# Kernel optimization log

Hardware: AMD Instinct MI355X
Metric: run time of the kernel (lower is better)

## Reference

```python
import jax, jax.numpy as jnp
import numpy as np
from jax import lax

B, T, VC, VB, DC, DB, H, C = 32, 512, 12000, 400000, 128, 128, 256, 32


def setup_inputs() -> dict:
    key = jax.random.key(0)
    ks = jax.random.split(key, 16)
    seq_len = jax.random.randint(ks[0], (B,), T // 2, T + 1)
    pos = jnp.arange(T)[None, :]
    mask = pos < seq_len[:, None]
    chars = jnp.where(mask, jax.random.randint(ks[1], (B, T), 1, VC), 0)
    bigrams = jnp.where(mask, jax.random.randint(ks[2], (B, T), 1, VB), 0)
    target = jnp.where(mask, jax.random.randint(ks[3], (B, T), 0, C), 0)
    s = lambda k, shape, scale: jax.random.normal(k, shape, jnp.float32) * scale
    D = DC + DB
    return dict(
        chars=chars, bigrams=bigrams, seq_len=seq_len, target=target,
        char_table=s(ks[4], (VC, DC), 0.1),
        bigram_table=s(ks[5], (VB, DB), 0.1),
        Wi_f=s(ks[6], (D, 4 * H), 0.05), Wh_f=s(ks[7], (H, 4 * H), 0.05),
        b_f=jnp.zeros((4 * H,), jnp.float32),
        Wi_b=s(ks[8], (D, 4 * H), 0.05), Wh_b=s(ks[9], (H, 4 * H), 0.05),
        b_b=jnp.zeros((4 * H,), jnp.float32),
        out_W=s(ks[10], (2 * H, C), 0.05), out_b=jnp.zeros((C,), jnp.float32),
        trans=s(ks[11], (C, C), 0.1),
        start_trans=s(ks[12], (C,), 0.1), end_trans=s(ks[13], (C,), 0.1),
    )


def _lstm_dir(x_t, m_t, Wi, Wh, b, reverse):
    # x_t: [T,B,D], m_t: [T,B,1]; masked carry emulates pack_padded_sequence
    Hh = Wh.shape[0]
    Bb = x_t.shape[1]

    def step(carry, inp):
        h, c = carry
        x, m = inp
        g = x @ Wi + h @ Wh + b  # [B,4H], torch gate order i,f,g,o
        i, f, gg, o = jnp.split(g, 4, axis=-1)
        c_new = jax.nn.sigmoid(f) * c + jax.nn.sigmoid(i) * jnp.tanh(gg)
        h_new = jax.nn.sigmoid(o) * jnp.tanh(c_new)
        h = jnp.where(m, h_new, h)
        c = jnp.where(m, c_new, c)
        return (h, c), h

    init = (jnp.zeros((Bb, Hh), x_t.dtype), jnp.zeros((Bb, Hh), x_t.dtype))
    _, hs = lax.scan(step, init, (x_t, m_t), reverse=reverse)
    return hs  # [T,B,H]


def reference(chars, bigrams, seq_len, target, char_table, bigram_table,
              Wi_f, Wh_f, b_f, Wi_b, Wh_b, b_b, out_W, out_b,
              trans, start_trans, end_trans):
    mask = chars != 0  # [B,T]
    emb = jnp.concatenate([char_table[chars], bigram_table[bigrams]], axis=-1)  # [B,T,D]
    x_t = jnp.transpose(emb, (1, 0, 2))          # [T,B,D]
    m_t = mask.T[..., None]                       # [T,B,1]
    hf = _lstm_dir(x_t, m_t, Wi_f, Wh_f, b_f, False)
    hb = _lstm_dir(x_t, m_t, Wi_b, Wh_b, b_b, True)
    feats = jnp.concatenate([hf, hb], axis=-1)    # [T,B,2H]
    logits = jax.nn.log_softmax(feats @ out_W + out_b, axis=-1)  # [T,B,C]
    mt = mask.T  # [T,B]

    # CRF normalizer (forward algorithm, include_start_end_trans=True)
    alpha0 = logits[0] + start_trans[None, :]

    def step(alpha, inp):
        emit, m = inp
        new = jax.nn.logsumexp(alpha[:, :, None] + trans[None] + emit[:, None, :], axis=1)
        return jnp.where(m[:, None], new, alpha), None

    alpha, _ = lax.scan(step, alpha0, (logits[1:], mt[1:]))
    normalizer = jax.nn.logsumexp(alpha + end_trans[None, :], axis=1)  # [B]

    # gold path score
    lg = jnp.transpose(logits, (1, 0, 2))  # [B,T,C]
    emit = jnp.where(mask, jnp.take_along_axis(lg, target[..., None], axis=-1)[..., 0], 0.0)
    tr = jnp.where(mask[:, 1:], trans[target[:, :-1], target[:, 1:]], 0.0)
    last_idx = jnp.sum(mask, axis=-1).astype(jnp.int32) - 1
    last_tag = jnp.take_along_axis(target, last_idx[:, None], axis=1)[:, 0]
    gold = emit.sum(-1) + tr.sum(-1) + start_trans[target[:, 0]] + end_trans[last_tag]

    return normalizer - gold  # per-sample CRF negative log-likelihood, [B]
```

## Files before the change

kernel.cpp:

```cpp
#include <hip/hip_runtime.h>
#include <cstdint>
#include <cstddef>

typedef unsigned short u16;
typedef unsigned int u32;
typedef unsigned long long u64;

typedef short short8 __attribute__((ext_vector_type(8)));
typedef float floatx4 __attribute__((ext_vector_type(4)));

#define O_EMB    0ull
#define O_XG     8388608ull
#define O_HS     75497472ull
#define O_HST    92274688ull
#define O_LOGITS 92340224ull
#define O_WIT    94437504ull
#define O_OUTW   95486080ull
#define O_FLAGS  95518848ull
#define WS_NEED  95520896ull

__device__ __forceinline__ u16 f2bf(float x) {
    u32 u = __float_as_uint(x);
    u += 0x7fffu + ((u >> 16) & 1u);
    return (u16)(u >> 16);
}
__device__ __forceinline__ float bf2f(u16 v) { return __uint_as_float(((u32)v) << 16); }
__device__ __forceinline__ float sigm(float x) { return 1.0f / (1.0f + __expf(-x)); }
__device__ __forceinline__ float tanh_f(float x) {
    x = fminf(30.0f, fmaxf(-30.0f, x));
    float e = __expf(-2.0f * x);
    return (1.0f - e) / (1.0f + e);
}

__global__ __launch_bounds__(256) void k_init(u32* hstate_u32, int* flags) {
    int i = blockIdx.x * 256 + threadIdx.x;
    if (i < 16384) hstate_u32[i] = 0u;
    if (i < 512) flags[i] = 0;
}

__global__ __launch_bounds__(256) void k0_prep(const float* __restrict__ Wi_f, const float* __restrict__ Wi_b,
                                               const float* __restrict__ out_W,
                                               u16* __restrict__ WiT, u16* __restrict__ outWb) {
    int id = blockIdx.x * 256 + threadIdx.x;
    if (id < 524288) {
        int d = id >> 18;
        int rem = id & 262143;
        int k = rem >> 10;
        int n = rem & 1023;
        const float* Wi = d ? Wi_b : Wi_f;
        WiT[(size_t)d * 262144 + (size_t)n * 256 + k] = f2bf(Wi[(size_t)k * 1024 + n]);
    } else {
        int id2 = id - 524288;
        outWb[id2] = f2bf(out_W[id2]);
    }
}

__global__ __launch_bounds__(256) void k1_embed(const int* __restrict__ chars, const int* __restrict__ bigrams,
                                                const float* __restrict__ ct, const float* __restrict__ bt,
                                                u16* __restrict__ emb) {
    int idx = blockIdx.x * 256 + threadIdx.x;
    int r = idx >> 7;
    int p2 = (idx & 127) << 1;
    int t = r >> 5, b = r & 31;
    const float* src;
    if (p2 < 128) src = ct + (size_t)chars[b * 512 + t] * 128 + p2;
    else          src = bt + (size_t)bigrams[b * 512 + t] * 128 + (p2 - 128);
    float2 v = *(const float2*)(const void*)src;
    u32 pk = (u32)f2bf(v.x) | ((u32)f2bf(v.y) << 16);
    *(u32*)(void*)(emb + (size_t)r * 256 + p2) = pk;
}

__global__ __launch_bounds__(256) void k2_gemm(const u16* __restrict__ emb, const u16* __restrict__ WiT,
                                               const float* __restrict__ b_f, const float* __restrict__ b_b,
                                               u16* __restrict__ xg) {
    int mbase = blockIdx.x * 64;
    int nbase = blockIdx.y * 64;
    int d = blockIdx.z;
    const u16* Bt = WiT + (size_t)d * 262144;
    const float* bias = d ? b_b : b_f;
    u16* xgd = xg + (size_t)d * 16777216ull;
    int tid = threadIdx.x;
    int wv = tid >> 6, l = tid & 63, lm = l & 15, lq = l >> 4;
    floatx4 acc[4] = {{0,0,0,0},{0,0,0,0},{0,0,0,0},{0,0,0,0}};
    int arow = mbase + wv * 16 + lm;
#pragma unroll
    for (int kc = 0; kc < 8; ++kc) {
        int k0 = kc * 32 + lq * 8;
        short8 a = *(const short8*)(const void*)(emb + (size_t)arow * 256 + k0);
#pragma unroll
        for (int nt = 0; nt < 4; ++nt) {
            short8 bb = *(const short8*)(const void*)(Bt + (size_t)(nbase + nt * 16 + lm) * 256 + k0);
            acc[nt] = __builtin_amdgcn_mfma_f32_16x16x32_bf16(a, bb, acc[nt], 0, 0, 0);
        }
    }
#pragma unroll
    for (int nt = 0; nt < 4; ++nt) {
        int n = nbase + nt * 16 + lm;
        float bv = bias[n];
#pragma unroll
        for (int r = 0; r < 4; ++r) {
            int rr = mbase + wv * 16 + lq * 4 + r;
            xgd[(size_t)rr * 1024 + n] = f2bf(acc[nt][r] + bv);
        }
    }
}

__global__ __launch_bounds__(256) void k3_lstm(const u16* __restrict__ xg, const float* __restrict__ Wh_f,
                                               const float* __restrict__ Wh_b, const int* __restrict__ seq_len,
                                               u16* __restrict__ hstate, u16* __restrict__ hs,
                                               int* __restrict__ flags) {
    int bid = blockIdx.x;
    int dir = bid >> 4;
    int w = bid & 15;
    const float* Wh = dir ? Wh_b : Wh_f;
    const u16* xgd = xg + (size_t)dir * 16777216ull;
    u16* hsd = hs + (size_t)dir * 4194304ull;
    __shared__ u16 lds_w[64 * 264];
    __shared__ float gate_lds[32 * 68];
    int tid = threadIdx.x;

    for (int it = 0; it < 64; ++it) {
        int e = it * 256 + tid;
        int p = e & 63;
        int k = e >> 6;
        int gcol = (p >> 4) * 256 + w * 16 + (p & 15);
        lds_w[p * 264 + k] = f2bf(Wh[(size_t)k * 1024 + gcol]);
    }
    int bcell = tid >> 3, uu = tid & 7, c0 = uu * 2;
    int L = seq_len[bcell];
    float cst0 = 0.0f, cst1 = 0.0f;
    int wv = tid >> 6, l = tid & 63, lm = l & 15, lq = l >> 4, mt = wv & 1, nh = wv >> 1;
    int* myflags = flags + dir * 256;
    __syncthreads();

    for (int s = 0; s < 512; ++s) {
        int t = dir ? (511 - s) : s;
        u32 xgv[4];
        const u16* xrow = xgd + ((size_t)(t * 32 + bcell)) * 1024 + w * 16 + c0;
#pragma unroll
        for (int g = 0; g < 4; ++g) xgv[g] = *(const u32*)(const void*)(xrow + g * 256);

        if (s > 0) {
            if (tid < 64) {
                for (;;) {
                    int v = (tid < 16)
                        ? __hip_atomic_load(&myflags[tid * 16], __ATOMIC_RELAXED, __HIP_MEMORY_SCOPE_AGENT)
                        : 0x7fffffff;
                    if (__ballot(v >= s) == ~0ull) break;
                    __builtin_amdgcn_s_sleep(1);
                }
            }
            __syncthreads();
            __builtin_amdgcn_sched_barrier(0);
        }
        const u64* hbq = (const u64*)(const void*)(hstate + ((size_t)(dir * 2 + (s & 1))) * 8192);
        int arowh = mt * 16 + lm;
        u64 aq[16];
#pragma unroll
        for (int kc = 0; kc < 8; ++kc) {
            size_t qi = (size_t)arowh * 64 + (size_t)kc * 8 + lq * 2;
            aq[2 * kc]     = __hip_atomic_load(hbq + qi,     __ATOMIC_RELAXED, __HIP_MEMORY_SCOPE_AGENT);
            aq[2 * kc + 1] = __hip_atomic_load(hbq + qi + 1, __ATOMIC_RELAXED, __HIP_MEMORY_SCOPE_AGENT);
        }
        floatx4 acc0 = {0,0,0,0}, acc1 = {0,0,0,0};
#pragma unroll
        for (int kc = 0; kc < 8; ++kc) {
            union { u64 q[2]; short8 s8; } ua;
            ua.q[0] = aq[2 * kc];
            ua.q[1] = aq[2 * kc + 1];
            int k0 = kc * 32 + lq * 8;
            short8 b0 = *(const short8*)(const void*)&lds_w[(nh * 32 + lm) * 264 + k0];
            acc0 = __builtin_amdgcn_mfma_f32_16x16x32_bf16(ua.s8, b0, acc0, 0, 0, 0);
            short8 b1 = *(const short8*)(const void*)&lds_w[(nh * 32 + 16 + lm) * 264 + k0];
            acc1 = __builtin_amdgcn_mfma_f32_16x16x32_bf16(ua.s8, b1, acc1, 0, 0, 0);
        }
#pragma unroll
        for (int r = 0; r < 4; ++r) {
            int b2 = mt * 16 + lq * 4 + r;
            gate_lds[b2 * 68 + nh * 32 + lm] = acc0[r];
            gate_lds[b2 * 68 + nh * 32 + 16 + lm] = acc1[r];
        }
        __syncthreads();
        float hv0, hv1;
#pragma unroll
        for (int r = 0; r < 2; ++r) {
            int cc = c0 + r;
            float gi = gate_lds[bcell * 68 + cc]      + bf2f((u16)(xgv[0] >> (16 * r)));
            float gf = gate_lds[bcell * 68 + 16 + cc] + bf2f((u16)(xgv[1] >> (16 * r)));
            float gg = gate_lds[bcell * 68 + 32 + cc] + bf2f((u16)(xgv[2] >> (16 * r)));
            float go = gate_lds[bcell * 68 + 48 + cc] + bf2f((u16)(xgv[3] >> (16 * r)));
            float ig = sigm(gi), fg = sigm(gf), gt = tanh_f(gg), og = sigm(go);
            float cs = r ? cst1 : cst0;
            float cn = fg * cs + ig * gt;
            float hn = og * tanh_f(cn);
            if (dir && t >= L) { cn = cs; hn = 0.0f; }
            if (r) { cst1 = cn; hv1 = hn; } else { cst0 = cn; hv0 = hn; }
        }
        u32 hpack = (u32)f2bf(hv0) | ((u32)f2bf(hv1) << 16);
        u32* hbn = (u32*)(void*)(hstate + ((size_t)(dir * 2 + ((s + 1) & 1))) * 8192 + bcell * 256 + w * 16 + c0);
        __hip_atomic_store(hbn, hpack, __ATOMIC_RELAXED, __HIP_MEMORY_SCOPE_AGENT);
        __syncthreads();
        if (tid == 0) __hip_atomic_store(&myflags[w * 16], s + 1, __ATOMIC_RELAXED, __HIP_MEMORY_SCOPE_AGENT);
        *(u32*)(void*)(hsd + ((size_t)(t * 32 + bcell)) * 256 + w * 16 + c0) = hpack;
    }
}

__global__ __launch_bounds__(256) void k4_proj(const u16* __restrict__ hs, const u16* __restrict__ outWb,
                                               const float* __restrict__ out_b, float* __restrict__ logits) {
    int r = blockIdx.x * 8 + (threadIdx.x >> 5);
    int n = threadIdx.x & 31;
    const u16* hf = hs + (size_t)r * 256;
    const u16* hbk = hs + 4194304ull + (size_t)r * 256;
    float acc = out_b[n];
#pragma unroll 4
    for (int k = 0; k < 256; k += 2) {
        u32 hv = *(const u32*)(const void*)(hf + k);
        acc += bf2f((u16)hv) * bf2f(outWb[k * 32 + n]);
        acc += bf2f((u16)(hv >> 16)) * bf2f(outWb[(k + 1) * 32 + n]);
    }
#pragma unroll 4
    for (int k = 0; k < 256; k += 2) {
        u32 hv = *(const u32*)(const void*)(hbk + k);
        acc += bf2f((u16)hv) * bf2f(outWb[(256 + k) * 32 + n]);
        acc += bf2f((u16)(hv >> 16)) * bf2f(outWb[(257 + k) * 32 + n]);
    }
    float m = acc;
#pragma unroll
    for (int d2 = 16; d2 >= 1; d2 >>= 1) m = fmaxf(m, __shfl_xor(m, d2, 32));
    float s = __expf(acc - m);
#pragma unroll
    for (int d2 = 16; d2 >= 1; d2 >>= 1) s += __shfl_xor(s, d2, 32);
    logits[(size_t)r * 32 + n] = acc - m - __logf(s);
}

__global__ __launch_bounds__(256) void k5_crf(const float* __restrict__ logits, const int* __restrict__ target,
                                              const int* __restrict__ seq_len, const float* __restrict__ trans,
                                              const float* __restrict__ start_trans, const float* __restrict__ end_trans,
                                              float* __restrict__ out) {
    int b = blockIdx.x;
    int tid = threadIdx.x;
    int L = seq_len[b];
    __shared__ float alpha[32];
    __shared__ float red[4];
    __shared__ float goldsh;

    float part = 0.0f;
    for (int t = tid; t < 512; t += 256) {
        if (t < L) {
            int tg = target[b * 512 + t];
            part += logits[((size_t)(t * 32 + b)) * 32 + tg];
            if (t >= 1) part += trans[target[b * 512 + t - 1] * 32 + tg];
        }
    }
#pragma unroll
    for (int d2 = 32; d2 >= 1; d2 >>= 1) part += __shfl_xor(part, d2, 64);
    if ((tid & 63) == 0) red[tid >> 6] = part;
    __syncthreads();
    if (tid == 0) {
        float g = red[0] + red[1] + red[2] + red[3];
        g += start_trans[target[b * 512]];
        g += end_trans[target[b * 512 + L - 1]];
        goldsh = g;
    }
    if (tid < 32) alpha[tid] = logits[(size_t)b * 32 + tid] + start_trans[tid];
    __syncthreads();

    int j = tid >> 3, uu = tid & 7;
    float tr4[4];
#pragma unroll
    for (int r = 0; r < 4; ++r) tr4[r] = trans[(uu * 4 + r) * 32 + j];
    float e_next = logits[((size_t)(32 + b)) * 32 + j];
    for (int t = 1; t < 512; ++t) {
        float e = e_next;
        if (t < 511) e_next = logits[((size_t)((t + 1) * 32 + b)) * 32 + j];
        float a0 = alpha[uu * 4 + 0] + tr4[0];
        float a1 = alpha[uu * 4 + 1] + tr4[1];
        float a2 = alpha[uu * 4 + 2] + tr4[2];
        float a3 = alpha[uu * 4 + 3] + tr4[3];
        float m = fmaxf(fmaxf(a0, a1), fmaxf(a2, a3));
#pragma unroll
        for (int d2 = 4; d2 >= 1; d2 >>= 1) m = fmaxf(m, __shfl_xor(m, d2, 8));
        float ss = __expf(a0 - m) + __expf(a1 - m) + __expf(a2 - m) + __expf(a3 - m);
#pragma unroll
        for (int d2 = 4; d2 >= 1; d2 >>= 1) ss += __shfl_xor(ss, d2, 8);
        float nv = e + m + __logf(ss);
        __syncthreads();
        if (uu == 0 && t < L) alpha[j] = nv;
        __syncthreads();
    }
    if (tid < 32) {
        float v = alpha[tid] + end_trans[tid];
        float m = v;
#pragma unroll
        for (int d2 = 16; d2 >= 1; d2 >>= 1) m = fmaxf(m, __shfl_xor(m, d2, 32));
        float s2 = __expf(v - m);
#pragma unroll
        for (int d2 = 16; d2 >= 1; d2 >>= 1) s2 += __shfl_xor(s2, d2, 32);
        if (tid == 0) out[b] = m + __logf(s2) - goldsh;
    }
}

extern "C" void kernel_launch(void* const* d_in, const int* in_sizes, int n_in,
                              void* d_out, int out_size, void* d_ws, size_t ws_size,
                              hipStream_t stream) {
    if (ws_size < WS_NEED) return;
    const int* chars = (const int*)d_in[0];
    const int* bigrams = (const int*)d_in[1];
    const int* seq_len = (const int*)d_in[2];
    const int* target = (const int*)d_in[3];
    const float* char_table = (const float*)d_in[4];
    const float* bigram_table = (const float*)d_in[5];
    const float* Wi_f = (const float*)d_in[6];
    const float* Wh_f = (const float*)d_in[7];
    const float* b_f = (const float*)d_in[8];
    const float* Wi_b = (const float*)d_in[9];
    const float* Wh_b = (const float*)d_in[10];
    const float* b_b = (const float*)d_in[11];
    const float* out_W = (const float*)d_in[12];
    const float* out_b = (const float*)d_in[13];
    const float* trans = (const float*)d_in[14];
    const float* start_trans = (const float*)d_in[15];
    const float* end_trans = (const float*)d_in[16];

    char* ws = (char*)d_ws;
    u16* emb = (u16*)(ws + O_EMB);
    u16* xg = (u16*)(ws + O_XG);
    u16* hs = (u16*)(ws + O_HS);
    u16* hst = (u16*)(ws + O_HST);
    float* logits = (float*)(ws + O_LOGITS);
    int* flags = (int*)(ws + O_FLAGS);
    u16* WiT = (u16*)(ws + O_WIT);
    u16* outWb = (u16*)(ws + O_OUTW);

    hipLaunchKernelGGL(k_init, dim3(64), dim3(256), 0, stream, (u32*)hst, flags);
    hipLaunchKernelGGL(k0_prep, dim3(2112), dim3(256), 0, stream, Wi_f, Wi_b, out_W, WiT, outWb);
    hipLaunchKernelGGL(k1_embed, dim3(8192), dim3(256), 0, stream, chars, bigrams, char_table, bigram_table, emb);
    hipLaunchKernelGGL(k2_gemm, dim3(256, 16, 2), dim3(256), 0, stream, emb, WiT, b_f, b_b, xg);
    hipLaunchKernelGGL(k3_lstm, dim3(32), dim3(256), 0, stream, xg, Wh_f, Wh_b, seq_len, hst, hs, flags);
    hipLaunchKernelGGL(k4_proj, dim3(2048), dim3(256), 0, stream, hs, outWb, out_b, logits);
    hipLaunchKernelGGL(k5_crf, dim3(32), dim3(256), 0, stream, logits, target, seq_len, trans, start_trans, end_trans,
                       (float*)d_out);
}
```

Before: 2.464 ms.

## Replace cross-block flag-synced LSTM with per-direction single-workgroup register-resident recurrence

The LSTM recurrence was split across 16 workgroups per direction that exchanged hidden state through global memory and spin-waited on atomic flags every timestep. It now runs as 4 workgroups of 1024 threads, one per direction and batch half. Each keeps the bf16 recurrent weights in registers, double-buffers h in LDS, and synchronises each step with a single workgroup barrier. The input-gate GEMM output is re-laid out as [t][gate-col][batch] so each thread reads its gates with a few 64-bit loads. Wh is pre-transposed to bf16 in the prep kernel and stored in the logits region, which is only overwritten later. This removes the global-memory handshake latency but uses only 4 CUs, with heavy register pressure from 32 short8 weight fragments per thread.

```diff
diff --git a/kernel.cpp b/kernel.cpp
--- a/kernel.cpp
+++ b/kernel.cpp
@@ -32,15 +32,11 @@
     return (1.0f - e) / (1.0f + e);
 }
 
-__global__ __launch_bounds__(256) void k_init(u32* hstate_u32, int* flags) {
-    int i = blockIdx.x * 256 + threadIdx.x;
-    if (i < 16384) hstate_u32[i] = 0u;
-    if (i < 512) flags[i] = 0;
-}
-
 __global__ __launch_bounds__(256) void k0_prep(const float* __restrict__ Wi_f, const float* __restrict__ Wi_b,
+                                               const float* __restrict__ Wh_f, const float* __restrict__ Wh_b,
                                                const float* __restrict__ out_W,
-                                               u16* __restrict__ WiT, u16* __restrict__ outWb) {
+                                               u16* __restrict__ WiT, u16* __restrict__ WhT,
+                                               u16* __restrict__ outWb) {
     int id = blockIdx.x * 256 + threadIdx.x;
     if (id < 524288) {
         int d = id >> 18;
@@ -49,9 +45,17 @@
         int n = rem & 1023;
         const float* Wi = d ? Wi_b : Wi_f;
         WiT[(size_t)d * 262144 + (size_t)n * 256 + k] = f2bf(Wi[(size_t)k * 1024 + n]);
-    } else {
+    } else if (id < 540672) {
         int id2 = id - 524288;
         outWb[id2] = f2bf(out_W[id2]);
+    } else {
+        int id2 = id - 540672;
+        int d = id2 >> 18;
+        int rem = id2 & 262143;
+        int k = rem >> 10;
+        int n = rem & 1023;
+        const float* Wh = d ? Wh_b : Wh_f;
+        WhT[(size_t)d * 262144 + (size_t)n * 256 + k] = f2bf(Wh[(size_t)k * 1024 + n]);
     }
 }
 
@@ -93,115 +97,94 @@
             acc[nt] = __builtin_amdgcn_mfma_f32_16x16x32_bf16(a, bb, acc[nt], 0, 0, 0);
         }
     }
+    int rr0 = mbase + wv * 16 + lq * 4;
+    int tt = rr0 >> 5, b0 = rr0 & 31;
 #pragma unroll
     for (int nt = 0; nt < 4; ++nt) {
         int n = nbase + nt * 16 + lm;
         float bv = bias[n];
-#pragma unroll
-        for (int r = 0; r < 4; ++r) {
-            int rr = mbase + wv * 16 + lq * 4 + r;
-            xgd[(size_t)rr * 1024 + n] = f2bf(acc[nt][r] + bv);
-        }
-    }
-}
-
-__global__ __launch_bounds__(256) void k3_lstm(const u16* __restrict__ xg, const float* __restrict__ Wh_f,
-                                               const float* __restrict__ Wh_b, const int* __restrict__ seq_len,
-                                               u16* __restrict__ hstate, u16* __restrict__ hs,
-                                               int* __restrict__ flags) {
+        u64 pk = (u64)f2bf(acc[nt][0] + bv)
+               | ((u64)f2bf(acc[nt][1] + bv) << 16)
+               | ((u64)f2bf(acc[nt][2] + bv) << 32)
+               | ((u64)f2bf(acc[nt][3] + bv) << 48);
+        *(u64*)(void*)(xgd + ((size_t)tt * 1024 + n) * 32 + b0) = pk;
+    }
+}
+
+__global__ __launch_bounds__(1024) void k3_lstm(const u16* __restrict__ xg, const u16* __restrict__ WhT,
+                                                const int* __restrict__ seq_len, u16* __restrict__ hs) {
     int bid = blockIdx.x;
-    int dir = bid >> 4;
-    int w = bid & 15;
-    const float* Wh = dir ? Wh_b : Wh_f;
+    int dir = bid >> 1;
+    int half = bid & 1;
     const u16* xgd = xg + (size_t)dir * 16777216ull;
+    const u16* whd = WhT + (size_t)dir * 262144ull;
     u16* hsd = hs + (size_t)dir * 4194304ull;
-    __shared__ u16 lds_w[64 * 264];
-    __shared__ float gate_lds[32 * 68];
+
+    __shared__ __align__(16) u16 h_all[2][21120];
+
     int tid = threadIdx.x;
-
-    for (int it = 0; it < 64; ++it) {
-        int e = it * 256 + tid;
-        int p = e & 63;
-        int k = e >> 6;
-        int gcol = (p >> 4) * 256 + w * 16 + (p & 15);
-        lds_w[p * 264 + k] = f2bf(Wh[(size_t)k * 1024 + gcol]);
-    }
-    int bcell = tid >> 3, uu = tid & 7, c0 = uu * 2;
-    int L = seq_len[bcell];
-    float cst0 = 0.0f, cst1 = 0.0f;
-    int wv = tid >> 6, l = tid & 63, lm = l & 15, lq = l >> 4, mt = wv & 1, nh = wv >> 1;
-    int* myflags = flags + dir * 256;
+    int wv = tid >> 6;
+    int l = tid & 63;
+    int lm = l & 15, lq = l >> 4;
+    int c_dim = wv * 16 + lm;
+
+    short8 whb[4][8];
+#pragma unroll
+    for (int g = 0; g < 4; ++g)
+#pragma unroll
+        for (int kc = 0; kc < 8; ++kc)
+            whb[g][kc] = *(const short8*)(const void*)(whd + (size_t)(g * 256 + c_dim) * 256 + kc * 32 + lq * 8);
+
+    float cst[4] = {0.f, 0.f, 0.f, 0.f};
+    int Lr[4];
+#pragma unroll
+    for (int r = 0; r < 4; ++r) Lr[r] = seq_len[half * 16 + lq * 4 + r];
+
+    for (int i = tid; i < 4224; i += 1024) h_all[0][i] = 0;
     __syncthreads();
+
+    const int aoff = lm * 264 + lq * 8;
+    const int hrow = lq * 4;
 
     for (int s = 0; s < 512; ++s) {
         int t = dir ? (511 - s) : s;
-        u32 xgv[4];
-        const u16* xrow = xgd + ((size_t)(t * 32 + bcell)) * 1024 + w * 16 + c0;
-#pragma unroll
-        for (int g = 0; g < 4; ++g) xgv[g] = *(const u32*)(const void*)(xrow + g * 256);
-
-        if (s > 0) {
-            if (tid < 64) {
-                for (;;) {
-                    int v = (tid < 16)
-                        ? __hip_atomic_load(&myflags[tid * 16], __ATOMIC_RELAXED, __HIP_MEMORY_SCOPE_AGENT)
-                        : 0x7fffffff;
-                    if (__ballot(v >= s) == ~0ull) break;
-                    __builtin_amdgcn_s_sleep(1);
-                }
-            }
-            __syncthreads();
-            __builtin_amdgcn_sched_barrier(0);
+        const u16* xbase = xgd + (size_t)t * 32768 + (size_t)c_dim * 32 + half * 16 + lq * 4;
+        u64 xq0 = *(const u64*)(const void*)(xbase);
+        u64 xq1 = *(const u64*)(const void*)(xbase + 8192);
+        u64 xq2 = *(const u64*)(const void*)(xbase + 16384);
+        u64 xq3 = *(const u64*)(const void*)(xbase + 24576);
+
+        const u16* hb = h_all[s & 1];
+        floatx4 acc0 = {0,0,0,0}, acc1 = {0,0,0,0}, acc2 = {0,0,0,0}, acc3 = {0,0,0,0};
+#pragma unroll
+        for (int kc = 0; kc < 8; ++kc) {
+            short8 a = *(const short8*)(const void*)(hb + aoff + kc * 32);
+            acc0 = __builtin_amdgcn_mfma_f32_16x16x32_bf16(a, whb[0][kc], acc0, 0, 0, 0);
+            acc1 = __builtin_amdgcn_mfma_f32_16x16x32_bf16(a, whb[1][kc], acc1, 0, 0, 0);
+            acc2 = __builtin_amdgcn_mfma_f32_16x16x32_bf16(a, whb[2][kc], acc2, 0, 0, 0);
+            acc3 = __builtin_amdgcn_mfma_f32_16x16x32_bf16(a, whb[3][kc], acc3, 0, 0, 0);
         }
-        const u64* hbq = (const u64*)(const void*)(hstate + ((size_t)(dir * 2 + (s & 1))) * 8192);
-        int arowh = mt * 16 + lm;
-        u64 aq[16];
-#pragma unroll
-        for (int kc = 0; kc < 8; ++kc) {
-            size_t qi = (size_t)arowh * 64 + (size_t)kc * 8 + lq * 2;
-            aq[2 * kc]     = __hip_atomic_load(hbq + qi,     __ATOMIC_RELAXED, __HIP_MEMORY_SCOPE_AGENT);
-            aq[2 * kc + 1] = __hip_atomic_load(hbq + qi + 1, __ATOMIC_RELAXED, __HIP_MEMORY_SCOPE_AGENT);
+
+        u16* hw = h_all[(s & 1) ^ 1];
+#pragma unroll
+        for (int r = 0; r < 4; ++r) {
+            float gi = acc0[r] + bf2f((u16)(xq0 >> (16 * r)));
+            float gf = acc1[r] + bf2f((u16)(xq1 >> (16 * r)));
+            float gg = acc2[r] + bf2f((u16)(xq2 >> (16 * r)));
+            float go = acc3[r] + bf2f((u16)(xq3 >> (16 * r)));
+            float ig = sigm(gi), fg = sigm(gf), gt = tanh_f(gg), og = sigm(go);
+            float cn = fg * cst[r] + ig * gt;
+            float hn = og * tanh_f(cn);
+            if (dir && t >= Lr[r]) { cn = cst[r]; hn = 0.0f; }
+            cst[r] = cn;
+            u16 hbf = f2bf(hn);
+            hw[(hrow + r) * 264 + c_dim] = hbf;
+            hsd[((size_t)(t * 32 + half * 16 + hrow + r)) * 256 + c_dim] = hbf;
         }
-        floatx4 acc0 = {0,0,0,0}, acc1 = {0,0,0,0};
-#pragma unroll
-        for (int kc = 0; kc < 8; ++kc) {
-            union { u64 q[2]; short8 s8; } ua;
-            ua.q[0] = aq[2 * kc];
-            ua.q[1] = aq[2 * kc + 1];
-            int k0 = kc * 32 + lq * 8;
-            short8 b0 = *(const short8*)(const void*)&lds_w[(nh * 32 + lm) * 264 + k0];
-            acc0 = __builtin_amdgcn_mfma_f32_16x16x32_bf16(ua.s8, b0, acc0, 0, 0, 0);
-            short8 b1 = *(const short8*)(const void*)&lds_w[(nh * 32 + 16 + lm) * 264 + k0];
-            acc1 = __builtin_amdgcn_mfma_f32_16x16x32_bf16(ua.s8, b1, acc1, 0, 0, 0);
-        }
-#pragma unroll
-        for (int r = 0; r < 4; ++r) {
-            int b2 = mt * 16 + lq * 4 + r;
-            gate_lds[b2 * 68 + nh * 32 + lm] = acc0[r];
-            gate_lds[b2 * 68 + nh * 32 + 16 + lm] = acc1[r];
-        }
-        __syncthreads();
-        float hv0, hv1;
-#pragma unroll
-        for (int r = 0; r < 2; ++r) {
-            int cc = c0 + r;
-            float gi = gate_lds[bcell * 68 + cc]      + bf2f((u16)(xgv[0] >> (16 * r)));
-            float gf = gate_lds[bcell * 68 + 16 + cc] + bf2f((u16)(xgv[1] >> (16 * r)));
-            float gg = gate_lds[bcell * 68 + 32 + cc] + bf2f((u16)(xgv[2] >> (16 * r)));
-            float go = gate_lds[bcell * 68 + 48 + cc] + bf2f((u16)(xgv[3] >> (16 * r)));
-            float ig = sigm(gi), fg = sigm(gf), gt = tanh_f(gg), og = sigm(go);
-            float cs = r ? cst1 : cst0;
-            float cn = fg * cs + ig * gt;
-            float hn = og * tanh_f(cn);
-            if (dir && t >= L) { cn = cs; hn = 0.0f; }
-            if (r) { cst1 = cn; hv1 = hn; } else { cst0 = cn; hv0 = hn; }
-        }
-        u32 hpack = (u32)f2bf(hv0) | ((u32)f2bf(hv1) << 16);
-        u32* hbn = (u32*)(void*)(hstate + ((size_t)(dir * 2 + ((s + 1) & 1))) * 8192 + bcell * 256 + w * 16 + c0);
-        __hip_atomic_store(hbn, hpack, __ATOMIC_RELAXED, __HIP_MEMORY_SCOPE_AGENT);
-        __syncthreads();
-        if (tid == 0) __hip_atomic_store(&myflags[w * 16], s + 1, __ATOMIC_RELAXED, __HIP_MEMORY_SCOPE_AGENT);
-        *(u32*)(void*)(hsd + ((size_t)(t * 32 + bcell)) * 256 + w * 16 + c0) = hpack;
+        asm volatile("s_waitcnt lgkmcnt(0)" ::: "memory");
+        __builtin_amdgcn_sched_barrier(0);
+        __builtin_amdgcn_s_barrier();
+        __builtin_amdgcn_sched_barrier(0);
     }
 }
 
@@ -326,17 +309,15 @@
     u16* emb = (u16*)(ws + O_EMB);
     u16* xg = (u16*)(ws + O_XG);
     u16* hs = (u16*)(ws + O_HS);
-    u16* hst = (u16*)(ws + O_HST);
     float* logits = (float*)(ws + O_LOGITS);
-    int* flags = (int*)(ws + O_FLAGS);
+    u16* WhT = (u16*)(ws + O_LOGITS);
     u16* WiT = (u16*)(ws + O_WIT);
     u16* outWb = (u16*)(ws + O_OUTW);
 
-    hipLaunchKernelGGL(k_init, dim3(64), dim3(256), 0, stream, (u32*)hst, flags);
-    hipLaunchKernelGGL(k0_prep, dim3(2112), dim3(256), 0, stream, Wi_f, Wi_b, out_W, WiT, outWb);
+    hipLaunchKernelGGL(k0_prep, dim3(4160), dim3(256), 0, stream, Wi_f, Wi_b, Wh_f, Wh_b, out_W, WiT, WhT, outWb);
     hipLaunchKernelGGL(k1_embed, dim3(8192), dim3(256), 0, stream, chars, bigrams, char_table, bigram_table, emb);
     hipLaunchKernelGGL(k2_gemm, dim3(256, 16, 2), dim3(256), 0, stream, emb, WiT, b_f, b_b, xg);
-    hipLaunchKernelGGL(k3_lstm, dim3(32), dim3(256), 0, stream, xg, Wh_f, Wh_b, seq_len, hst, hs, flags);
+    hipLaunchKernelGGL(k3_lstm, dim3(4), dim3(1024), 0, stream, xg, WhT, seq_len, hs);
     hipLaunchKernelGGL(k4_proj, dim3(2048), dim3(256), 0, stream, hs, outWb, out_b, logits);
     hipLaunchKernelGGL(k5_crf, dim3(32), dim3(256), 0, stream, logits, target, seq_len, trans, start_trans, end_trans,
                        (float*)d_out);
```

Result: slower. 5.344 ms (+116.9%).
